# Kernel optimization log

Measured on AMD Instinct MI355X. Metric: run time of the kernel, lower is better.

Reference implementation:

```python
import jax, jax.numpy as jnp
import numpy as np

D_IN, D_H, BATCH = 4096, 512, 8192


def _layernorm(x, g, b, eps=1e-5):
    mu = jnp.mean(x, axis=-1, keepdims=True)
    var = jnp.var(x, axis=-1, keepdims=True)
    return (x - mu) * jax.lax.rsqrt(var + eps) * g + b


def setup_inputs() -> dict:
    key = jax.random.key(0)
    ks = jax.random.split(key, 10)
    x = jax.random.normal(ks[0], (BATCH, D_IN), jnp.float32)
    h = jax.random.normal(ks[1], (BATCH, D_H), jnp.float32)
    s1 = 1.0 / np.sqrt(D_IN + D_H)
    W1 = jax.random.uniform(ks[2], (D_IN + D_H, D_H), jnp.float32, -s1, s1)
    b1 = jnp.zeros((D_H,), jnp.float32)
    ln1_g = jnp.ones((D_H,), jnp.float32)
    ln1_b = jnp.zeros((D_H,), jnp.float32)
    s2 = 1.0 / np.sqrt(D_H)
    W2 = jax.random.uniform(ks[3], (D_H, 3 * D_H), jnp.float32, -s2, s2)
    b2 = jnp.zeros((3 * D_H,), jnp.float32)
    base_tau = jnp.ones((D_H,), jnp.float32)  # time_constant_init = 1.0
    base_A = jax.random.normal(ks[4], (D_H, D_H), jnp.float32) * 0.1
    idx = jnp.arange(D_H)
    base_A = base_A.at[idx, idx].set(-0.5)
    base_B = jax.random.normal(ks[5], (D_IN, D_H), jnp.float32) * 0.1
    hn_g = jnp.ones((D_H,), jnp.float32)
    hn_b = jnp.zeros((D_H,), jnp.float32)
    return {"x": x, "h": h, "W1": W1, "b1": b1, "ln1_g": ln1_g, "ln1_b": ln1_b,
            "W2": W2, "b2": b2, "base_tau": base_tau, "base_A": base_A,
            "base_B": base_B, "hn_g": hn_g, "hn_b": hn_b}


def reference(x, h, W1, b1, ln1_g, ln1_b, W2, b2, base_tau, base_A, base_B, hn_g, hn_b):
    dt = 0.1
    # time_net hypernetwork
    xh = jnp.concatenate([x, h], axis=-1)                 # [B, D_IN+D_H]
    t = _layernorm(xh @ W1 + b1, ln1_g, ln1_b)
    t = jax.nn.gelu(t, approximate=False)
    params = t @ W2 + b2                                  # [B, 3*D_H]
    tau_s, A_s, B_s = jnp.split(params, 3, axis=-1)
    tau = base_tau * (jax.nn.sigmoid(tau_s) * 2.0)        # [B, D_H]
    A_row = 1.0 + 0.5 * jnp.tanh(A_s)                     # per-sample row scale of A
    B_col = 1.0 + 0.5 * jnp.tanh(B_s)                     # per-sample col scale of B
    # A[b] = base_A * A_row[b][:,None]; h @ A[b].T == (h @ base_A.T) * A_row[b]
    recurrent = (h @ base_A.T) * A_row                    # [B, D_H]
    # B[b] = base_B * B_col[b][None,:]; x @ B[b] == (x @ base_B) * B_col[b]
    input_term = (x @ base_B) * B_col                     # [B, D_H]
    dhdt = -h / (tau + 1e-8) + jnp.tanh(recurrent + input_term)
    new_h = _layernorm(h + dt * dhdt, hn_g, hn_b)
    return new_h
```

## Files before the change

kernel.cpp:

```cpp
#include <hip/hip_runtime.h>

#define BATCH 8192
#define DIN 4096
#define DH 512

typedef float f32x4 __attribute__((ext_vector_type(4)));
typedef float f32x2 __attribute__((ext_vector_type(2)));
typedef short s16x8 __attribute__((ext_vector_type(8)));
typedef unsigned short u16x2 __attribute__((ext_vector_type(2)));
typedef unsigned short u16x4 __attribute__((ext_vector_type(4)));
typedef unsigned short u16x8 __attribute__((ext_vector_type(8)));

static __device__ __forceinline__ unsigned short f2bf(float f) {
  unsigned int u = __float_as_uint(f);
  u += 0x7FFFu + ((u >> 16) & 1u);
  return (unsigned short)(u >> 16);
}
static __device__ __forceinline__ float bf2f(unsigned short s) {
  return __uint_as_float(((unsigned int)s) << 16);
}

typedef const __attribute__((address_space(1))) unsigned int* gas_ptr;
typedef __attribute__((address_space(3))) unsigned int* las_ptr;
static __device__ __forceinline__ void gl_lds16(const unsigned short* g, unsigned short* l) {
  __builtin_amdgcn_global_load_lds((gas_ptr)g, (las_ptr)l, 16, 0, 0);
}

static __device__ __forceinline__ void transpose_body(
    const float* __restrict__ in, int C,
    unsigned short* __restrict__ out, int ldo, int row_off,
    int bx, int by, float (*tl)[33])
{
  const int tid = threadIdx.x;
  const int tx = tid & 31, ty = tid >> 5;
  const int c0 = bx * 32, r0 = by * 32;
#pragma unroll
  for (int i = 0; i < 4; i++)
    tl[ty + 8 * i][tx] = in[(size_t)(r0 + ty + 8 * i) * C + c0 + tx];
  __syncthreads();
#pragma unroll
  for (int i = 0; i < 4; i++)
    out[(size_t)(row_off + c0 + ty + 8 * i) * ldo + r0 + tx] = f2bf(tl[tx][ty + 8 * i]);
}

__global__ __launch_bounds__(256) void prep_all_k(
    const float* __restrict__ x, unsigned short* __restrict__ xbf,
    const float* __restrict__ h, unsigned short* __restrict__ hbf,
    const float* __restrict__ base_A, unsigned short* __restrict__ Abf,
    const float* __restrict__ W1, const float* __restrict__ base_B,
    unsigned short* __restrict__ BTcat,
    const float* __restrict__ W2, unsigned short* __restrict__ W2T)
{
  __shared__ float tl[32][33];
  const int b = blockIdx.x;
  const int tid = threadIdx.x;
  const int KC = DIN + DH;
  if (b < 32768) {
    const int i = (b * 256 + tid) * 4;
    f32x4 v = *(const f32x4*)(x + i);
    u16x4 p = { f2bf(v[0]), f2bf(v[1]), f2bf(v[2]), f2bf(v[3]) };
    *(u16x4*)(xbf + i) = p;
  } else if (b < 36864) {
    const int i = ((b - 32768) * 256 + tid) * 4;
    f32x4 v = *(const f32x4*)(h + i);
    u16x4 p = { f2bf(v[0]), f2bf(v[1]), f2bf(v[2]), f2bf(v[3]) };
    *(u16x4*)(hbf + i) = p;
  } else if (b < 37120) {
    const int i = ((b - 36864) * 256 + tid) * 4;
    f32x4 v = *(const f32x4*)(base_A + i);
    u16x4 p = { f2bf(v[0]), f2bf(v[1]), f2bf(v[2]), f2bf(v[3]) };
    *(u16x4*)(Abf + i) = p;
  } else if (b < 39424) {
    const int bb = b - 37120;
    transpose_body(W1, DH, BTcat, KC, 0, bb & 15, bb >> 4, tl);
  } else if (b < 41472) {
    const int bb = b - 39424;
    transpose_body(base_B, DH, BTcat, KC, DH, bb & 15, bb >> 4, tl);
  } else if (b < 41600) {
    const int gid = (b - 41472) * 256 + tid;
    const int row = gid >> 6, c = (gid & 63) * 8;
    u16x8 z = { 0, 0, 0, 0, 0, 0, 0, 0 };
    *(u16x8*)(BTcat + (size_t)(DH + row) * KC + DIN + c) = z;
  } else {
    const int bb = b - 41600;
    transpose_body(W2, 3 * DH, W2T, DH, 0, bb % 48, bb / 48, tl);
  }
}

template<int EPI>
static __device__ __forceinline__ void gemm2_engine(
    const unsigned short* __restrict__ A0, int lda0, int K0,
    const unsigned short* __restrict__ A1, int lda1,
    const unsigned short* __restrict__ BT, int ldb,
    unsigned short* __restrict__ C0, int ldc,
    unsigned short* __restrict__ C1,
    const float* __restrict__ bias,
    const float* __restrict__ base_tau,
    int mb, int nb, int K, char* smem)
{
  unsigned short* As = (unsigned short*)smem;
  unsigned short* Bs = (unsigned short*)(smem + 32768);
  float* red = (float*)smem;

  const int tid = threadIdx.x;
  const int lane = tid & 63;
  const int wid = tid >> 6;
  const int grp = wid >> 2;
  const int wg  = wid & 3;
  const int wm = (wg >> 1) * 64;
  const int wn = (wg & 1) * 64;
  const int srow = lane >> 2;
  const int scol = ((lane & 3) ^ ((lane >> 3) & 3)) * 8;
  const int fr = lane & 15;
  const int fk = ((lane >> 4) ^ ((lane >> 1) & 3)) * 8;
  const int NT2 = K / 64;

  f32x4 acc[4][4];
#pragma unroll
  for (int i = 0; i < 4; i++)
#pragma unroll
    for (int j = 0; j < 4; j++)
      acc[i][j] = (f32x4){ 0.f, 0.f, 0.f, 0.f };

  auto STAGE_A = [&](int buf, int per) {
    const int tk = 2 * per + grp;
    const int k0 = tk * 32;
    const bool s0 = (k0 < K0);
    const unsigned short* Ab = s0 ? A0 : A1;
    const int ld = s0 ? lda0 : lda1;
    const int ko = (s0 ? k0 : k0 - K0) + scol;
    unsigned short* ab = As + (grp * 2 + buf) * 4096 + (32 * wg) * 32;
#pragma unroll
    for (int c = 0; c < 2; c++) {
      const int r = 32 * wg + c * 16 + srow;
      gl_lds16(Ab + (size_t)(mb + r) * ld + ko, ab + c * 16 * 32);
    }
  };
  auto STAGE_B = [&](int buf, int per) {
    const int tk = 2 * per + grp;
    const int k0 = tk * 32;
    unsigned short* bb = Bs + (grp * 2 + buf) * 4096 + (32 * wg) * 32;
#pragma unroll
    for (int c = 0; c < 2; c++) {
      const int r = 32 * wg + c * 16 + srow;
      gl_lds16(BT + (size_t)(nb + r) * ldb + k0 + scol, bb + c * 16 * 32);
    }
  };

  STAGE_A(0, 0);
  STAGE_B(0, 0);
  asm volatile("s_waitcnt vmcnt(0)" ::: "memory");
  __builtin_amdgcn_s_barrier();

  int buf = 0;
  for (int t = 0; t < NT2; t++) {
    const unsigned short* ar = As + (grp * 2 + buf) * 4096;
    const unsigned short* br = Bs + (grp * 2 + buf) * 4096;
    s16x8 af[4], bv[4];
#pragma unroll
    for (int mi = 0; mi < 4; mi++)
      af[mi] = *(const s16x8*)(ar + (wm + mi * 16 + fr) * 32 + fk);
    bv[0] = *(const s16x8*)(br + (wn + fr) * 32 + fk);

#pragma unroll
    for (int p = 0; p < 4; p++) {
      if (p < 3)
        bv[p + 1] = *(const s16x8*)(br + (wn + (p + 1) * 16 + fr) * 32 + fk);
      if (p == 0 && t + 1 < NT2) STAGE_A(buf ^ 1, t + 1);
      if (p == 1 && t + 1 < NT2) STAGE_B(buf ^ 1, t + 1);

      __builtin_amdgcn_s_setprio(1);
#pragma unroll
      for (int mi = 0; mi < 4; mi++)
        acc[mi][p] = __builtin_amdgcn_mfma_f32_16x16x32_bf16(
            af[mi], bv[p], acc[mi][p], 0, 0, 0);
      __builtin_amdgcn_s_setprio(0);

      if (p == 3) {
        asm volatile("s_waitcnt vmcnt(0) lgkmcnt(0)" ::: "memory");
        __builtin_amdgcn_sched_barrier(0);
      }
      __builtin_amdgcn_s_barrier();
    }
    buf ^= 1;
  }

  if (grp == 1) {
#pragma unroll
    for (int mi = 0; mi < 4; mi++)
#pragma unroll
      for (int ni = 0; ni < 4; ni++)
        *(f32x4*)(red + (((wg * 4 + mi) * 4 + ni) * 64 + lane) * 4) = acc[mi][ni];
  }
  __syncthreads();
  if (grp != 0) return;

  const int rb = (lane >> 4) * 4;
#pragma unroll
  for (int mi = 0; mi < 4; mi++) {
#pragma unroll
    for (int ni = 0; ni < 4; ni++) {
      f32x4 o = *(const f32x4*)(red + (((wg * 4 + mi) * 4 + ni) * 64 + lane) * 4);
      acc[mi][ni] += o;
#pragma unroll
      for (int r = 0; r < 4; r++) {
        const int row = mb + wm + mi * 16 + rb + r;
        const int col = nb + wn + ni * 16 + fr;
        float v = acc[mi][ni][r];
        if (EPI == 3) {
          if (col < DH) C0[(size_t)row * DH + col] = f2bf(v + bias[col]);
          else          C1[(size_t)row * DH + (col - DH)] = f2bf(v);
        } else if (EPI == 2) {
          C0[(size_t)row * ldc + col] = f2bf(v);
        } else if (EPI == 1) {
          v += bias[col];
          if ((col >> 9) == 0) {
            const float s = 1.0f / (1.0f + expf(-v));
            v = 1.0f / (base_tau[col & (DH - 1)] * 2.0f * s + 1e-8f);
          } else {
            v = 1.0f + 0.5f * tanhf(v);
          }
          C0[(size_t)row * ldc + col] = f2bf(v);
        }
      }
    }
  }
}

__global__ __launch_bounds__(512, 4) void fused_gemm_k(
    const unsigned short* __restrict__ xbf,
    const unsigned short* __restrict__ hbf,
    const unsigned short* __restrict__ BTcat,
    unsigned short* __restrict__ pre1,
    unsigned short* __restrict__ rawB,
    const float* __restrict__ b1)
{
  __shared__ __align__(16) char smem[65536];
  const int cpx = gridDim.x >> 3;
  const int virt = (blockIdx.x & 7) * cpx + (blockIdx.x >> 3);
  const int mb = (virt & 63) * 128;
  const int nb = (virt >> 6) * 128;
  gemm2_engine<3>(xbf, DIN, DIN, hbf, DH, BTcat, DIN + DH,
                  pre1, DH, rawB, b1, nullptr, mb, nb, DIN + DH, smem);
}

__global__ __launch_bounds__(512, 4) void tail_gemm_k(
    const unsigned short* __restrict__ hbf,
    const unsigned short* __restrict__ Abf,
    const unsigned short* __restrict__ tbf,
    const unsigned short* __restrict__ W2T,
    unsigned short* __restrict__ rawA,
    unsigned short* __restrict__ scales,
    const float* __restrict__ b2,
    const float* __restrict__ base_tau)
{
  __shared__ __align__(16) char smem[65536];
  const int b = blockIdx.x;
  if (b < 768) {
    const int mb = (b & 63) * 128, nb = (b >> 6) * 128;
    gemm2_engine<1>(tbf, DH, DH, nullptr, 0, W2T, DH,
                    scales, 3 * DH, nullptr, b2, base_tau, mb, nb, DH, smem);
  } else {
    const int b2i = b - 768;
    const int mb = (b2i & 63) * 128, nb = (b2i >> 6) * 128;
    gemm2_engine<2>(hbf, DH, DH, nullptr, 0, Abf, DH,
                    rawA, DH, nullptr, nullptr, nullptr, mb, nb, DH, smem);
  }
}

__device__ __forceinline__ float block_sum256(float v, float* red) {
#pragma unroll
  for (int m = 32; m >= 1; m >>= 1) v += __shfl_xor(v, m, 64);
  __syncthreads();
  if ((threadIdx.x & 63) == 0) red[threadIdx.x >> 6] = v;
  __syncthreads();
  return red[0] + red[1] + red[2] + red[3];
}

__global__ __launch_bounds__(256) void ln_gelu_k(
    const unsigned short* __restrict__ pre,
    const float* __restrict__ g, const float* __restrict__ b,
    unsigned short* __restrict__ t)
{
  __shared__ float red[4];
  const int row = blockIdx.x;
  const int c = threadIdx.x * 2;
  const size_t ro = (size_t)row * DH;
  u16x2 raw = *(const u16x2*)(pre + ro + c);
  const float v0 = bf2f(raw[0]), v1 = bf2f(raw[1]);
  const float mu = block_sum256(v0 + v1, red) * (1.0f / DH);
  const float d0 = v0 - mu, d1 = v1 - mu;
  const float var = block_sum256(d0 * d0 + d1 * d1, red) * (1.0f / DH);
  const float inv = rsqrtf(var + 1e-5f);
  const float y0 = d0 * inv * g[c] + b[c];
  const float y1 = d1 * inv * g[c + 1] + b[c + 1];
  u16x2 o = { f2bf(0.5f * y0 * (1.0f + erff(y0 * 0.70710678118f))),
              f2bf(0.5f * y1 * (1.0f + erff(y1 * 0.70710678118f))) };
  *(u16x2*)(t + ro + c) = o;
}

__global__ __launch_bounds__(256) void final_k(
    const float* __restrict__ h,
    const unsigned short* __restrict__ rawA,
    const unsigned short* __restrict__ rawB,
    const unsigned short* __restrict__ scales,
    const float* __restrict__ hn_g, const float* __restrict__ hn_b,
    float* __restrict__ out)
{
  __shared__ float red[4];
  const int row = blockIdx.x;
  const int c = threadIdx.x * 2;
  const size_t ro = (size_t)row * DH;
  f32x2 hv = *(const f32x2*)(h + ro + c);
  u16x2 ra = *(const u16x2*)(rawA + ro + c);
  u16x2 rb = *(const u16x2*)(rawB + ro + c);
  const unsigned short* sc = scales + (size_t)row * (3 * DH);
  u16x2 ti  = *(const u16x2*)(sc + c);
  u16x2 arw = *(const u16x2*)(sc + DH + c);
  u16x2 bcl = *(const u16x2*)(sc + 2 * DH + c);
  const float u0 = hv[0] + 0.1f * (-hv[0] * bf2f(ti[0])
                 + tanhf(bf2f(ra[0]) * bf2f(arw[0]) + bf2f(rb[0]) * bf2f(bcl[0])));
  const float u1 = hv[1] + 0.1f * (-hv[1] * bf2f(ti[1])
                 + tanhf(bf2f(ra[1]) * bf2f(arw[1]) + bf2f(rb[1]) * bf2f(bcl[1])));
  const float mu = block_sum256(u0 + u1, red) * (1.0f / DH);
  const float d0 = u0 - mu, d1 = u1 - mu;
  const float var = block_sum256(d0 * d0 + d1 * d1, red) * (1.0f / DH);
  const float inv = rsqrtf(var + 1e-5f);
  f32x2 o = { d0 * inv * hn_g[c] + hn_b[c],
              d1 * inv * hn_g[c + 1] + hn_b[c + 1] };
  *(f32x2*)(out + ro + c) = o;
}

extern "C" void kernel_launch(void* const* d_in, const int* in_sizes, int n_in,
                              void* d_out, int out_size, void* d_ws, size_t ws_size,
                              hipStream_t stream)
{
  const float* x        = (const float*)d_in[0];
  const float* h        = (const float*)d_in[1];
  const float* W1       = (const float*)d_in[2];
  const float* b1       = (const float*)d_in[3];
  const float* ln1_g    = (const float*)d_in[4];
  const float* ln1_b    = (const float*)d_in[5];
  const float* W2       = (const float*)d_in[6];
  const float* b2       = (const float*)d_in[7];
  const float* base_tau = (const float*)d_in[8];
  const float* base_A   = (const float*)d_in[9];
  const float* base_B   = (const float*)d_in[10];
  const float* hn_g     = (const float*)d_in[11];
  const float* hn_b     = (const float*)d_in[12];

  char* w = (char*)d_ws;
  unsigned short* xbf    = (unsigned short*)(w);
  unsigned short* hbf    = (unsigned short*)(w + 67108864);
  unsigned short* BTcat  = (unsigned short*)(w + 75497472);
  unsigned short* tbf    = (unsigned short*)(w + 75497472);
  unsigned short* W2T    = (unsigned short*)(w + 84934656);
  unsigned short* Abf    = (unsigned short*)(w + 86507520);
  unsigned short* pre1   = (unsigned short*)(w + 87031808);
  unsigned short* rawA   = (unsigned short*)(w + 87031808);
  unsigned short* rawB   = (unsigned short*)(w + 95420416);
  unsigned short* scales = (unsigned short*)(w + 103809024);

  prep_all_k<<<42368, 256, 0, stream>>>(x, xbf, h, hbf, base_A, Abf,
                                        W1, base_B, BTcat, W2, W2T);

  fused_gemm_k<<<512, 512, 0, stream>>>(xbf, hbf, BTcat, pre1, rawB, b1);
  ln_gelu_k<<<BATCH, 256, 0, stream>>>(pre1, ln1_g, ln1_b, tbf);
  tail_gemm_k<<<1024, 512, 0, stream>>>(hbf, Abf, tbf, W2T, rawA, scales, b2, base_tau);
  final_k<<<BATCH, 256, 0, stream>>>(h, rawA, rawB, scales, hn_g, hn_b, (float*)d_out);
}
```

Measured before the change: 213.9 us.

## Use 128x256 output tiles without split-K in the fused first GEMM

Adds a new GEMM engine for the main x|h projection. Each 512-thread block now computes a 128x256 output tile with all 8 waves tiling the output, replacing the previous 128x128 tile whose two wave groups split K and were reduced through LDS. This halves the grid to 256 blocks, cuts repeated loads of the A operand and removes the LDS reduction pass. The cost is fewer blocks than compute units to fill the GPU (a single wave of work), more serial K iterations per block, and the occupancy hint dropped from launch bounds.

```diff
diff --git a/kernel.cpp b/kernel.cpp
--- a/kernel.cpp
+++ b/kernel.cpp
@@ -88,7 +88,7 @@
 }
 
 template<int EPI>
-static __device__ __forceinline__ void gemm2_engine(
+static __device__ __forceinline__ void gemm3_engine(
     const unsigned short* __restrict__ A0, int lda0, int K0,
     const unsigned short* __restrict__ A1, int lda1,
     const unsigned short* __restrict__ BT, int ldb,
@@ -99,21 +99,19 @@
     int mb, int nb, int K, char* smem)
 {
   unsigned short* As = (unsigned short*)smem;
-  unsigned short* Bs = (unsigned short*)(smem + 32768);
-  float* red = (float*)smem;
+  unsigned short* Bs = (unsigned short*)(smem + 16384);
 
   const int tid = threadIdx.x;
   const int lane = tid & 63;
   const int wid = tid >> 6;
-  const int grp = wid >> 2;
-  const int wg  = wid & 3;
-  const int wm = (wg >> 1) * 64;
-  const int wn = (wg & 1) * 64;
+  const int wm = (wid >> 2) * 64;
+  const int wn = (wid & 3) * 64;
   const int srow = lane >> 2;
   const int scol = ((lane & 3) ^ ((lane >> 3) & 3)) * 8;
   const int fr = lane & 15;
   const int fk = ((lane >> 4) ^ ((lane >> 1) & 3)) * 8;
-  const int NT2 = K / 64;
+  const int NT = K / 32;
+  const int cw = wid * 3;
 
   f32x4 acc[4][4];
 #pragma unroll
@@ -122,86 +120,73 @@
     for (int j = 0; j < 4; j++)
       acc[i][j] = (f32x4){ 0.f, 0.f, 0.f, 0.f };
 
-  auto STAGE_A = [&](int buf, int per) {
-    const int tk = 2 * per + grp;
-    const int k0 = tk * 32;
-    const bool s0 = (k0 < K0);
-    const unsigned short* Ab = s0 ? A0 : A1;
-    const int ld = s0 ? lda0 : lda1;
-    const int ko = (s0 ? k0 : k0 - K0) + scol;
-    unsigned short* ab = As + (grp * 2 + buf) * 4096 + (32 * wg) * 32;
-#pragma unroll
-    for (int c = 0; c < 2; c++) {
-      const int r = 32 * wg + c * 16 + srow;
-      gl_lds16(Ab + (size_t)(mb + r) * ld + ko, ab + c * 16 * 32);
+  auto STAGE1 = [&](int buf, int t, int j) {
+    const int c = cw + j;
+    const int k0 = t * 32;
+    if (c < 8) {
+      const bool s0 = (k0 < K0);
+      const unsigned short* Ab = s0 ? A0 : A1;
+      const int ld = s0 ? lda0 : lda1;
+      const int ko = (s0 ? k0 : k0 - K0) + scol;
+      gl_lds16(Ab + (size_t)(mb + c * 16 + srow) * ld + ko,
+               As + buf * 4096 + c * 512);
+    } else {
+      gl_lds16(BT + (size_t)(nb + (c - 8) * 16 + srow) * ldb + k0 + scol,
+               Bs + buf * 8192 + (c - 8) * 512);
     }
   };
-  auto STAGE_B = [&](int buf, int per) {
-    const int tk = 2 * per + grp;
-    const int k0 = tk * 32;
-    unsigned short* bb = Bs + (grp * 2 + buf) * 4096 + (32 * wg) * 32;
-#pragma unroll
-    for (int c = 0; c < 2; c++) {
-      const int r = 32 * wg + c * 16 + srow;
-      gl_lds16(BT + (size_t)(nb + r) * ldb + k0 + scol, bb + c * 16 * 32);
-    }
-  };
-
-  STAGE_A(0, 0);
-  STAGE_B(0, 0);
+
+  STAGE1(0, 0, 0); STAGE1(0, 0, 1); STAGE1(0, 0, 2);
   asm volatile("s_waitcnt vmcnt(0)" ::: "memory");
   __builtin_amdgcn_s_barrier();
 
   int buf = 0;
-  for (int t = 0; t < NT2; t++) {
-    const unsigned short* ar = As + (grp * 2 + buf) * 4096;
-    const unsigned short* br = Bs + (grp * 2 + buf) * 4096;
-    s16x8 af[4], bv[4];
+  for (int t = 0; t < NT; t++) {
+    const unsigned short* ar = As + buf * 4096;
+    const unsigned short* br = Bs + buf * 8192;
+    s16x8 af[4], bv0, bv1, bv2, bv3;
 #pragma unroll
     for (int mi = 0; mi < 4; mi++)
       af[mi] = *(const s16x8*)(ar + (wm + mi * 16 + fr) * 32 + fk);
-    bv[0] = *(const s16x8*)(br + (wn + fr) * 32 + fk);
-
-#pragma unroll
-    for (int p = 0; p < 4; p++) {
-      if (p < 3)
-        bv[p + 1] = *(const s16x8*)(br + (wn + (p + 1) * 16 + fr) * 32 + fk);
-      if (p == 0 && t + 1 < NT2) STAGE_A(buf ^ 1, t + 1);
-      if (p == 1 && t + 1 < NT2) STAGE_B(buf ^ 1, t + 1);
-
-      __builtin_amdgcn_s_setprio(1);
-#pragma unroll
-      for (int mi = 0; mi < 4; mi++)
-        acc[mi][p] = __builtin_amdgcn_mfma_f32_16x16x32_bf16(
-            af[mi], bv[p], acc[mi][p], 0, 0, 0);
-      __builtin_amdgcn_s_setprio(0);
-
-      if (p == 3) {
-        asm volatile("s_waitcnt vmcnt(0) lgkmcnt(0)" ::: "memory");
-        __builtin_amdgcn_sched_barrier(0);
-      }
-      __builtin_amdgcn_s_barrier();
-    }
+    bv0 = *(const s16x8*)(br + (wn + 0 * 16 + fr) * 32 + fk);
+    bv1 = *(const s16x8*)(br + (wn + 1 * 16 + fr) * 32 + fk);
+
+    if (t + 1 < NT) { STAGE1(buf ^ 1, t + 1, 0); STAGE1(buf ^ 1, t + 1, 1); }
+
+    __builtin_amdgcn_s_setprio(1);
+#pragma unroll
+    for (int mi = 0; mi < 4; mi++)
+      acc[mi][0] = __builtin_amdgcn_mfma_f32_16x16x32_bf16(af[mi], bv0, acc[mi][0], 0, 0, 0);
+#pragma unroll
+    for (int mi = 0; mi < 4; mi++)
+      acc[mi][1] = __builtin_amdgcn_mfma_f32_16x16x32_bf16(af[mi], bv1, acc[mi][1], 0, 0, 0);
+    __builtin_amdgcn_s_setprio(0);
+    __builtin_amdgcn_s_barrier();
+
+    bv2 = *(const s16x8*)(br + (wn + 2 * 16 + fr) * 32 + fk);
+    bv3 = *(const s16x8*)(br + (wn + 3 * 16 + fr) * 32 + fk);
+    if (t + 1 < NT) STAGE1(buf ^ 1, t + 1, 2);
+
+    __builtin_amdgcn_s_setprio(1);
+#pragma unroll
+    for (int mi = 0; mi < 4; mi++)
+      acc[mi][2] = __builtin_amdgcn_mfma_f32_16x16x32_bf16(af[mi], bv2, acc[mi][2], 0, 0, 0);
+#pragma unroll
+    for (int mi = 0; mi < 4; mi++)
+      acc[mi][3] = __builtin_amdgcn_mfma_f32_16x16x32_bf16(af[mi], bv3, acc[mi][3], 0, 0, 0);
+    __builtin_amdgcn_s_setprio(0);
+
+    asm volatile("s_waitcnt vmcnt(0) lgkmcnt(0)" ::: "memory");
+    __builtin_amdgcn_sched_barrier(0);
+    __builtin_amdgcn_s_barrier();
     buf ^= 1;
   }
 
-  if (grp == 1) {
-#pragma unroll
-    for (int mi = 0; mi < 4; mi++)
-#pragma unroll
-      for (int ni = 0; ni < 4; ni++)
-        *(f32x4*)(red + (((wg * 4 + mi) * 4 + ni) * 64 + lane) * 4) = acc[mi][ni];
-  }
-  __syncthreads();
-  if (grp != 0) return;
-
   const int rb = (lane >> 4) * 4;
 #pragma unroll
   for (int mi = 0; mi < 4; mi++) {
 #pragma unroll
     for (int ni = 0; ni < 4; ni++) {
-      f32x4 o = *(const f32x4*)(red + (((wg * 4 + mi) * 4 + ni) * 64 + lane) * 4);
-      acc[mi][ni] += o;
 #pragma unroll
       for (int r = 0; r < 4; r++) {
         const int row = mb + wm + mi * 16 + rb + r;
@@ -227,7 +212,142 @@
   }
 }
 
-__global__ __launch_bounds__(512, 4) void fused_gemm_k(
+template<int EPI>
+static __device__ __forceinline__ void gemm2_engine(
+    const unsigned short* __restrict__ A0, int lda0, int K0,
+    const unsigned short* __restrict__ A1, int lda1,
+    const unsigned short* __restrict__ BT, int ldb,
+    unsigned short* __restrict__ C0, int ldc,
+    unsigned short* __restrict__ C1,
+    const float* __restrict__ bias,
+    const float* __restrict__ base_tau,
+    int mb, int nb, int K, char* smem)
+{
+  unsigned short* As = (unsigned short*)smem;
+  unsigned short* Bs = (unsigned short*)(smem + 32768);
+  float* red = (float*)smem;
+
+  const int tid = threadIdx.x;
+  const int lane = tid & 63;
+  const int wid = tid >> 6;
+  const int grp = wid >> 2;
+  const int wg  = wid & 3;
+  const int wm = (wg >> 1) * 64;
+  const int wn = (wg & 1) * 64;
+  const int srow = lane >> 2;
+  const int scol = ((lane & 3) ^ ((lane >> 3) & 3)) * 8;
+  const int fr = lane & 15;
+  const int fk = ((lane >> 4) ^ ((lane >> 1) & 3)) * 8;
+  const int NT2 = K / 64;
+
+  f32x4 acc[4][4];
+#pragma unroll
+  for (int i = 0; i < 4; i++)
+#pragma unroll
+    for (int j = 0; j < 4; j++)
+      acc[i][j] = (f32x4){ 0.f, 0.f, 0.f, 0.f };
+
+  auto STAGE_A = [&](int buf, int per) {
+    const int k0 = (2 * per + grp) * 32;
+    const bool s0 = (k0 < K0);
+    const unsigned short* Ab = s0 ? A0 : A1;
+    const int ld = s0 ? lda0 : lda1;
+    const int ko = (s0 ? k0 : k0 - K0) + scol;
+    unsigned short* ab = As + (grp * 2 + buf) * 4096 + (32 * wg) * 32;
+#pragma unroll
+    for (int c = 0; c < 2; c++) {
+      const int r = 32 * wg + c * 16 + srow;
+      gl_lds16(Ab + (size_t)(mb + r) * ld + ko, ab + c * 16 * 32);
+    }
+  };
+  auto STAGE_B = [&](int buf, int per) {
+    const int k0 = (2 * per + grp) * 32;
+    unsigned short* bb = Bs + (grp * 2 + buf) * 4096 + (32 * wg) * 32;
+#pragma unroll
+    for (int c = 0; c < 2; c++) {
+      const int r = 32 * wg + c * 16 + srow;
+      gl_lds16(BT + (size_t)(nb + r) * ldb + k0 + scol, bb + c * 16 * 32);
+    }
+  };
+
+  STAGE_A(0, 0);
+  STAGE_B(0, 0);
+  asm volatile("s_waitcnt vmcnt(0)" ::: "memory");
+  __builtin_amdgcn_s_barrier();
+
+  int buf = 0;
+  for (int t = 0; t < NT2; t++) {
+    const unsigned short* ar = As + (grp * 2 + buf) * 4096;
+    const unsigned short* br = Bs + (grp * 2 + buf) * 4096;
+    s16x8 af[4], bv[4];
+#pragma unroll
+    for (int mi = 0; mi < 4; mi++)
+      af[mi] = *(const s16x8*)(ar + (wm + mi * 16 + fr) * 32 + fk);
+    bv[0] = *(const s16x8*)(br + (wn + fr) * 32 + fk);
+
+#pragma unroll
+    for (int p = 0; p < 4; p++) {
+      if (p < 3)
+        bv[p + 1] = *(const s16x8*)(br + (wn + (p + 1) * 16 + fr) * 32 + fk);
+      if (p == 0 && t + 1 < NT2) STAGE_A(buf ^ 1, t + 1);
+      if (p == 1 && t + 1 < NT2) STAGE_B(buf ^ 1, t + 1);
+
+      __builtin_amdgcn_s_setprio(1);
+#pragma unroll
+      for (int mi = 0; mi < 4; mi++)
+        acc[mi][p] = __builtin_amdgcn_mfma_f32_16x16x32_bf16(
+            af[mi], bv[p], acc[mi][p], 0, 0, 0);
+      __builtin_amdgcn_s_setprio(0);
+
+      if (p == 3) {
+        asm volatile("s_waitcnt vmcnt(0) lgkmcnt(0)" ::: "memory");
+        __builtin_amdgcn_sched_barrier(0);
+      }
+      __builtin_amdgcn_s_barrier();
+    }
+    buf ^= 1;
+  }
+
+  if (grp == 1) {
+#pragma unroll
+    for (int mi = 0; mi < 4; mi++)
+#pragma unroll
+      for (int ni = 0; ni < 4; ni++)
+        *(f32x4*)(red + (((wg * 4 + mi) * 4 + ni) * 64 + lane) * 4) = acc[mi][ni];
+  }
+  __syncthreads();
+  if (grp != 0) return;
+
+  const int rb = (lane >> 4) * 4;
+#pragma unroll
+  for (int mi = 0; mi < 4; mi++) {
+#pragma unroll
+    for (int ni = 0; ni < 4; ni++) {
+      f32x4 o = *(const f32x4*)(red + (((wg * 4 + mi) * 4 + ni) * 64 + lane) * 4);
+      acc[mi][ni] += o;
+#pragma unroll
+      for (int r = 0; r < 4; r++) {
+        const int row = mb + wm + mi * 16 + rb + r;
+        const int col = nb + wn + ni * 16 + fr;
+        float v = acc[mi][ni][r];
+        if (EPI == 2) {
+          C0[(size_t)row * ldc + col] = f2bf(v);
+        } else if (EPI == 1) {
+          v += bias[col];
+          if ((col >> 9) == 0) {
+            const float s = 1.0f / (1.0f + expf(-v));
+            v = 1.0f / (base_tau[col & (DH - 1)] * 2.0f * s + 1e-8f);
+          } else {
+            v = 1.0f + 0.5f * tanhf(v);
+          }
+          C0[(size_t)row * ldc + col] = f2bf(v);
+        }
+      }
+    }
+  }
+}
+
+__global__ __launch_bounds__(512) void fused_gemm_k(
     const unsigned short* __restrict__ xbf,
     const unsigned short* __restrict__ hbf,
     const unsigned short* __restrict__ BTcat,
@@ -235,12 +355,12 @@
     unsigned short* __restrict__ rawB,
     const float* __restrict__ b1)
 {
-  __shared__ __align__(16) char smem[65536];
+  __shared__ __align__(16) char smem[49152];
   const int cpx = gridDim.x >> 3;
   const int virt = (blockIdx.x & 7) * cpx + (blockIdx.x >> 3);
   const int mb = (virt & 63) * 128;
-  const int nb = (virt >> 6) * 128;
-  gemm2_engine<3>(xbf, DIN, DIN, hbf, DH, BTcat, DIN + DH,
+  const int nb = (virt >> 6) * 256;
+  gemm3_engine<3>(xbf, DIN, DIN, hbf, DH, BTcat, DIN + DH,
                   pre1, DH, rawB, b1, nullptr, mb, nb, DIN + DH, smem);
 }
 
@@ -364,7 +484,7 @@
   prep_all_k<<<42368, 256, 0, stream>>>(x, xbf, h, hbf, base_A, Abf,
                                         W1, base_B, BTcat, W2, W2T);
 
-  fused_gemm_k<<<512, 512, 0, stream>>>(xbf, hbf, BTcat, pre1, rawB, b1);
+  fused_gemm_k<<<256, 512, 0, stream>>>(xbf, hbf, BTcat, pre1, rawB, b1);
   ln_gelu_k<<<BATCH, 256, 0, stream>>>(pre1, ln1_g, ln1_b, tbf);
   tail_gemm_k<<<1024, 512, 0, stream>>>(hbf, Abf, tbf, W2T, rawA, scales, b2, base_tau);
   final_k<<<BATCH, 256, 0, stream>>>(h, rawA, rawB, scales, hn_g, hn_b, (float*)d_out);
```

Result: slower. 239.3 us (+11.9%).
